# Kernel tuning notes

Measured on AMD Instinct MI355X. Metric: run time of the kernel, lower is better.

The kernel has to match this reference:

```python
import jax, jax.numpy as jnp
import numpy as np

V, E, H, O, S, N = 32000, 256, 512, 32000, 128, 256

def setup_inputs() -> dict:
    key = jax.random.key(0)
    ks = jax.random.split(key, 12)
    s = 0.05
    return {
        'x': jax.random.randint(ks[0], (N, 1), 0, V),
        'encoder_outputs': jax.random.normal(ks[1], (N, S, 2 * H), jnp.float32),
        'hidden': jax.random.normal(ks[2], (1, N, H), jnp.float32),
        'cell': jax.random.normal(ks[3], (1, N, H), jnp.float32),
        'emb': jax.random.normal(ks[4], (V, E), jnp.float32) * s,
        'W_energy': jax.random.normal(ks[5], (1, 3 * H), jnp.float32) * s,
        'b_energy': jnp.zeros((1,), jnp.float32),
        'W_ih': jax.random.normal(ks[6], (4 * H, E + 2 * H), jnp.float32) * s,
        'W_hh': jax.random.normal(ks[7], (4 * H, H), jnp.float32) * s,
        'b_ih': jnp.zeros((4 * H,), jnp.float32),
        'b_hh': jnp.zeros((4 * H,), jnp.float32),
        'W_out': jax.random.normal(ks[8], (O, H), jnp.float32) * s,
        'b_out': jnp.zeros((O,), jnp.float32),
    }

def reference(x, encoder_outputs, hidden, cell, emb, W_energy, b_energy,
              W_ih, W_hh, b_ih, b_hh, W_out, b_out):
    # Dropout is identity at inference (eval mode).
    embedding = emb[x]                      # [N,1,E]
    n, s, _ = encoder_outputs.shape
    h = hidden[0]                            # [N,H] (num_layers==1)
    h_rep = jnp.broadcast_to(h[:, None, :], (n, s, h.shape[-1]))  # [N,S,H]
    feat = jnp.concatenate([h_rep, encoder_outputs], axis=-1)     # [N,S,3H]
    energy = jax.nn.relu(feat @ W_energy.T + b_energy)            # [N,S,1]
    attention = jax.nn.softmax(energy, axis=1)                    # softmax over seq
    context = jnp.einsum('nsk,nsl->nkl', attention, encoder_outputs)  # [N,1,2H]
    lstm_in = jnp.concatenate([context, embedding], axis=-1)[:, 0, :]  # [N,E+2H]
    gates = lstm_in @ W_ih.T + b_ih + h @ W_hh.T + b_hh           # [N,4H]
    i, f, g, o = jnp.split(gates, 4, axis=-1)                     # torch gate order
    i, f, o = jax.nn.sigmoid(i), jax.nn.sigmoid(f), jax.nn.sigmoid(o)
    g = jnp.tanh(g)
    c_new = f * cell[0] + i * g
    h_new = o * jnp.tanh(c_new)
    outputs = h_new[:, None, :]                                   # [N,1,H]
    predictions = outputs @ W_out.T + b_out                       # [N,1,O]
    return predictions, h_new[None], c_new[None]
```

## Files before the change

kernel.cpp:

```cpp
#include <hip/hip_runtime.h>
#include <hip/hip_bf16.h>

#define N_ 256
#define S_ 128
#define H_ 512
#define E_ 256
#define O_ 32000
#define KZ 1792
#define GJ 2048
#define KSPLIT 4
#define KCHUNK 448
#define SSPLIT 4

typedef __attribute__((ext_vector_type(8))) short sv8;
typedef __attribute__((ext_vector_type(4))) float fv4;

__device__ __forceinline__ unsigned short f2bf(float f) {
  return __builtin_bit_cast(unsigned short, __float2bfloat16(f));
}

__device__ __forceinline__ sv8 pack8(fv4 a, fv4 b) {
  sv8 r;
  r[0] = (short)f2bf(a[0]); r[1] = (short)f2bf(a[1]);
  r[2] = (short)f2bf(a[2]); r[3] = (short)f2bf(a[3]);
  r[4] = (short)f2bf(b[0]); r[5] = (short)f2bf(b[1]);
  r[6] = (short)f2bf(b[2]); r[7] = (short)f2bf(b[3]);
  return r;
}

__global__ __launch_bounds__(256) void k_conv_wg(
    const float* __restrict__ Wih, const float* __restrict__ Whh,
    unsigned short* __restrict__ Wgbf)
{
  const int j = blockIdx.x;
  const int t = threadIdx.x;
  sv8* dst = (sv8*)(Wgbf + (size_t)j * KZ);
  if (t < 160) {
    const fv4* src = (const fv4*)(Wih + (size_t)j * 1280);
    dst[t] = pack8(src[2 * t], src[2 * t + 1]);
  } else if (t < 224) {
    const fv4* src = (const fv4*)(Whh + (size_t)j * 512);
    dst[t] = pack8(src[2 * (t - 160)], src[2 * (t - 160) + 1]);
  }
}

__global__ __launch_bounds__(512) void k_attn_part(
    const float* __restrict__ eo, const float* __restrict__ hid,
    const float* __restrict__ We, const float* __restrict__ be,
    float* __restrict__ pctx, float* __restrict__ pml)
{
  const int n = blockIdx.x;
  const int q = blockIdx.y;
  const int t = threadIdx.x;
  const int w = t >> 6;
  const int l = t & 63;

  __shared__ float s_red[8];
  __shared__ float s_m[8], s_l[8];
  __shared__ float s_ctx[8][1024];

  float hv = hid[(size_t)n * H_ + t] * We[t];
  #pragma unroll
  for (int off = 32; off >= 1; off >>= 1) hv += __shfl_xor(hv, off);
  if (l == 0) s_red[w] = hv;
  __syncthreads();
  float hWe = be[0];
  #pragma unroll
  for (int i = 0; i < 8; ++i) hWe += s_red[i];

  fv4 we0, we1, we2, we3;
  {
    const fv4* wp = (const fv4*)(We + H_);
    we0 = wp[l]; we1 = wp[l + 64]; we2 = wp[l + 128]; we3 = wp[l + 192];
  }

  float m = 0.f, lsum = 0.f;
  fv4 c0 = {0,0,0,0}, c1 = {0,0,0,0}, c2 = {0,0,0,0}, c3 = {0,0,0,0};
  const float* eob = eo + ((size_t)n * S_ + q * 32 + w * 4) * 1024;
  #pragma unroll 2
  for (int i = 0; i < 4; ++i) {
    const fv4* p = (const fv4*)(eob + (size_t)i * 1024);
    fv4 v0 = p[l], v1 = p[l + 64], v2 = p[l + 128], v3 = p[l + 192];
    float d = 0.f;
    #pragma unroll
    for (int c = 0; c < 4; ++c)
      d += v0[c]*we0[c] + v1[c]*we1[c] + v2[c]*we2[c] + v3[c]*we3[c];
    #pragma unroll
    for (int off = 32; off >= 1; off >>= 1) d += __shfl_xor(d, off);
    const float e  = fmaxf(d + hWe, 0.f);
    const float mn = fmaxf(m, e);
    const float sc = __expf(m - mn);
    const float pp = __expf(e - mn);
    lsum = lsum * sc + pp;
    #pragma unroll
    for (int c = 0; c < 4; ++c) {
      c0[c] = c0[c]*sc + pp*v0[c];
      c1[c] = c1[c]*sc + pp*v1[c];
      c2[c] = c2[c]*sc + pp*v2[c];
      c3[c] = c3[c]*sc + pp*v3[c];
    }
    m = mn;
  }
  if (l == 0) { s_m[w] = m; s_l[w] = lsum; }
  {
    fv4* sc_ = (fv4*)s_ctx[w];
    sc_[l] = c0; sc_[l+64] = c1; sc_[l+128] = c2; sc_[l+192] = c3;
  }
  __syncthreads();

  float M = s_m[0];
  #pragma unroll
  for (int i = 1; i < 8; ++i) M = fmaxf(M, s_m[i]);
  float wgt[8]; float L = 0.f;
  #pragma unroll
  for (int i = 0; i < 8; ++i) { wgt[i] = __expf(s_m[i] - M); L += wgt[i] * s_l[i]; }

  float* pc = pctx + ((size_t)(n * SSPLIT + q)) * 1024;
  for (int k = t; k < 1024; k += 512) {
    float acc = 0.f;
    #pragma unroll
    for (int i = 0; i < 8; ++i) acc += wgt[i] * s_ctx[i][k];
    pc[k] = acc;
  }
  if (t == 0) {
    pml[(n * SSPLIT + q) * 2 + 0] = M;
    pml[(n * SSPLIT + q) * 2 + 1] = L;
  }
}

__global__ __launch_bounds__(256) void k_attn_fin(
    const int* __restrict__ x, const float* __restrict__ emb,
    const float* __restrict__ hid, const float* __restrict__ pctx,
    const float* __restrict__ pml, unsigned short* __restrict__ z)
{
  const int n = blockIdx.x;
  const int t = threadIdx.x;
  float mq[SSPLIT], lq[SSPLIT];
  #pragma unroll
  for (int q = 0; q < SSPLIT; ++q) {
    mq[q] = pml[(n * SSPLIT + q) * 2 + 0];
    lq[q] = pml[(n * SSPLIT + q) * 2 + 1];
  }
  float M = mq[0];
  #pragma unroll
  for (int q = 1; q < SSPLIT; ++q) M = fmaxf(M, mq[q]);
  float wq[SSPLIT], L = 0.f;
  #pragma unroll
  for (int q = 0; q < SSPLIT; ++q) { wq[q] = __expf(mq[q] - M); L += wq[q] * lq[q]; }
  const float rL = 1.f / L;

  const fv4* p0 = (const fv4*)(pctx + (size_t)n * (SSPLIT * 1024));
  fv4 s = {0,0,0,0};
  #pragma unroll
  for (int q = 0; q < SSPLIT; ++q) {
    const fv4 v = p0[q * 256 + t];
    #pragma unroll
    for (int c = 0; c < 4; ++c) s[c] += wq[q] * v[c];
  }
  unsigned short* zr = z + (size_t)n * KZ;
  ushort4 o;
  o.x = f2bf(s[0] * rL);
  o.y = f2bf(s[1] * rL);
  o.z = f2bf(s[2] * rL);
  o.w = f2bf(s[3] * rL);
  *(ushort4*)(zr + 4*t) = o;

  zr[1024 + t] = f2bf(emb[(size_t)x[n] * E_ + t]);
  zr[1280 + t] = f2bf(hid[(size_t)n * H_ + t]);
  zr[1536 + t] = f2bf(hid[(size_t)n * H_ + 256 + t]);
}

__global__ __launch_bounds__(256) void k_gates(
    const unsigned short* __restrict__ z, const unsigned short* __restrict__ Wgbf,
    float* __restrict__ part)
{
  const int j0 = blockIdx.x * 64;
  const int n0 = blockIdx.y * 64;
  const int kc = blockIdx.z * KCHUNK;
  const int t = threadIdx.x;
  const int w = t >> 6, l = t & 63;
  const int lr = l & 15, lg = l >> 4;
  const int jb = j0 + w * 16 + lr;

  const unsigned short* arow = z + kc + 8 * lg;
  const unsigned short* wrow = Wgbf + (size_t)jb * KZ + kc + 8 * lg;

  fv4 acc[4] = {{0,0,0,0},{0,0,0,0},{0,0,0,0},{0,0,0,0}};
  #pragma unroll
  for (int s = 0; s < 14; ++s) {
    const sv8 bf = *(const sv8*)(wrow + s * 32);
    #pragma unroll
    for (int f = 0; f < 4; ++f) {
      const sv8 af = *(const sv8*)(arow + (size_t)(n0 + f*16 + lr) * KZ + s * 32);
      acc[f] = __builtin_amdgcn_mfma_f32_16x16x32_bf16(af, bf, acc[f], 0, 0, 0);
    }
  }
  float* pp = part + (size_t)blockIdx.z * (N_ * GJ);
  #pragma unroll
  for (int f = 0; f < 4; ++f) {
    #pragma unroll
    for (int r = 0; r < 4; ++r)
      pp[(size_t)(n0 + f*16 + lg*4 + r) * GJ + jb] = acc[f][r];
  }
}

__global__ __launch_bounds__(256) void k_lstm(
    const float* __restrict__ part, const float* __restrict__ cell,
    const float* __restrict__ bih, const float* __restrict__ bhh,
    float* __restrict__ hout, float* __restrict__ cout,
    unsigned short* __restrict__ hbf)
{
  const int tid = blockIdx.x * 256 + threadIdx.x;
  const int n = tid >> 9, hh = tid & 511;
  const size_t base = (size_t)n * GJ;
  float ig = bih[hh]        + bhh[hh];
  float fg = bih[512 + hh]  + bhh[512 + hh];
  float gg = bih[1024 + hh] + bhh[1024 + hh];
  float og = bih[1536 + hh] + bhh[1536 + hh];
  #pragma unroll
  for (int k = 0; k < KSPLIT; ++k) {
    const float* p = part + (size_t)k * (N_ * GJ) + base;
    ig += p[hh];
    fg += p[512 + hh];
    gg += p[1024 + hh];
    og += p[1536 + hh];
  }
  ig = 1.f / (1.f + __expf(-ig));
  fg = 1.f / (1.f + __expf(-fg));
  og = 1.f / (1.f + __expf(-og));
  gg = tanhf(gg);
  const float c = fg * cell[tid] + ig * gg;
  const float h = og * tanhf(c);
  cout[tid] = c;
  hout[tid] = h;
  hbf[tid] = f2bf(h);
}

__global__ __launch_bounds__(512, 2) void k_pred(
    const unsigned short* __restrict__ hbf, const float* __restrict__ Wout,
    const float* __restrict__ bout, float* __restrict__ pred)
{
  __shared__ unsigned short Blds[64 * 512];
  const int o0 = blockIdx.x * 64;
  const int t = threadIdx.x;

  #pragma unroll
  for (int i = 0; i < 8; ++i) {
    const int g = t + i * 512;
    const int row = g >> 6, c = g & 63;
    const fv4* src = (const fv4*)(Wout + (size_t)(o0 + row) * H_ + c * 8);
    const sv8 v = pack8(src[0], src[1]);
    *(sv8*)((char*)Blds + row * 1024 + ((c * 16) ^ ((row & 7) << 4))) = v;
  }
  __syncthreads();

  const int w = t >> 6, l = t & 63;
  const int lr = l & 15, lg = l >> 4;
  const int nr = w * 32;

  fv4 acc[2][4] = {};
  #pragma unroll
  for (int kk = 0; kk < 16; ++kk) {
    sv8 a[2];
    #pragma unroll
    for (int f = 0; f < 2; ++f)
      a[f] = *(const sv8*)(hbf + (size_t)(nr + f*16 + lr) * H_ + kk*32 + 8*lg);
    #pragma unroll
    for (int fo = 0; fo < 4; ++fo) {
      const int row = fo * 16 + lr;
      const sv8 b = *(const sv8*)((const char*)Blds + row * 1024 +
                                  ((kk*64 + lg*16) ^ ((row & 7) << 4)));
      #pragma unroll
      for (int f = 0; f < 2; ++f)
        acc[f][fo] = __builtin_amdgcn_mfma_f32_16x16x32_bf16(a[f], b, acc[f][fo], 0, 0, 0);
    }
  }
  #pragma unroll
  for (int fo = 0; fo < 4; ++fo) {
    const int oo = o0 + fo*16 + lr;
    const float bo = bout[oo];
    #pragma unroll
    for (int f = 0; f < 2; ++f) {
      #pragma unroll
      for (int r = 0; r < 4; ++r)
        pred[(size_t)(nr + f*16 + lg*4 + r) * O_ + oo] = acc[f][fo][r] + bo;
    }
  }
}

extern "C" void kernel_launch(void* const* d_in, const int* in_sizes, int n_in,
                              void* d_out, int out_size, void* d_ws, size_t ws_size,
                              hipStream_t stream) {
  const int*   x    = (const int*)  d_in[0];
  const float* eo   = (const float*)d_in[1];
  const float* hid  = (const float*)d_in[2];
  const float* cell = (const float*)d_in[3];
  const float* emb  = (const float*)d_in[4];
  const float* We   = (const float*)d_in[5];
  const float* be   = (const float*)d_in[6];
  const float* Wih  = (const float*)d_in[7];
  const float* Whh  = (const float*)d_in[8];
  const float* bih  = (const float*)d_in[9];
  const float* bhh  = (const float*)d_in[10];
  const float* Wout = (const float*)d_in[11];
  const float* bout = (const float*)d_in[12];

  float* pred = (float*)d_out;
  float* hout = pred + (size_t)N_ * O_;
  float* cout = hout + (size_t)N_ * H_;

  unsigned short* z    = (unsigned short*)d_ws;
  unsigned short* hbf  = z + (size_t)N_ * KZ;
  float* part = (float*)(hbf + (size_t)N_ * H_);
  float* pctx = part + (size_t)KSPLIT * N_ * GJ;
  float* pml  = pctx + (size_t)N_ * SSPLIT * 1024;
  unsigned short* Wgbf = (unsigned short*)(pml + 2048);

  k_conv_wg  <<<GJ, 256, 0, stream>>>(Wih, Whh, Wgbf);
  k_attn_part<<<dim3(256, SSPLIT), 512, 0, stream>>>(eo, hid, We, be, pctx, pml);
  k_attn_fin <<<256, 256, 0, stream>>>(x, emb, hid, pctx, pml, z);
  k_gates<<<dim3(32, 4, KSPLIT), 256, 0, stream>>>(z, Wgbf, part);
  k_lstm <<<512, 256, 0, stream>>>(part, cell, bih, bhh, hout, cout, hbf);
  k_pred <<<500, 512, 0, stream>>>(hbf, Wout, bout, pred);
}
```

Before: 92.16 us.

## Merge weight conversion and attention into one kernel with full-sequence blocks

Three launches (weight bf16 conversion, split attention partials, attention finalize) become one kernel. blockIdx.y selects either the attention path or the weight conversion path, which now runs as a grid-stride loop. Each attention block uses 1024 threads covering all 128 sequence positions, so the partial context/max/sum round trip through global memory and a launch disappear. In exchange, the attention grid drops from 1024 to 256 blocks, and each block needs 64KB of shared memory, which may reduce occupancy and parallelism for the bandwidth-heavy encoder read.

```diff
diff --git a/kernel.cpp b/kernel.cpp
--- a/kernel.cpp
+++ b/kernel.cpp
@@ -10,7 +10,6 @@
 #define GJ 2048
 #define KSPLIT 4
 #define KCHUNK 448
-#define SSPLIT 4
 
 typedef __attribute__((ext_vector_type(8))) short sv8;
 typedef __attribute__((ext_vector_type(4))) float fv4;
@@ -28,38 +27,40 @@
   return r;
 }
 
-__global__ __launch_bounds__(256) void k_conv_wg(
+__global__ __launch_bounds__(1024) void k_attn(
+    const int* __restrict__ x, const float* __restrict__ eo,
+    const float* __restrict__ hid, const float* __restrict__ emb,
+    const float* __restrict__ We, const float* __restrict__ be,
     const float* __restrict__ Wih, const float* __restrict__ Whh,
-    unsigned short* __restrict__ Wgbf)
-{
-  const int j = blockIdx.x;
-  const int t = threadIdx.x;
-  sv8* dst = (sv8*)(Wgbf + (size_t)j * KZ);
-  if (t < 160) {
-    const fv4* src = (const fv4*)(Wih + (size_t)j * 1280);
-    dst[t] = pack8(src[2 * t], src[2 * t + 1]);
-  } else if (t < 224) {
-    const fv4* src = (const fv4*)(Whh + (size_t)j * 512);
-    dst[t] = pack8(src[2 * (t - 160)], src[2 * (t - 160) + 1]);
-  }
-}
-
-__global__ __launch_bounds__(512) void k_attn_part(
-    const float* __restrict__ eo, const float* __restrict__ hid,
-    const float* __restrict__ We, const float* __restrict__ be,
-    float* __restrict__ pctx, float* __restrict__ pml)
-{
+    unsigned short* __restrict__ Wgbf, unsigned short* __restrict__ z)
+{
+  if (blockIdx.y == 1) {
+    const int tid = blockIdx.x * 1024 + threadIdx.x;
+    for (int g = tid; g < 2048 * 224; g += 256 * 1024) {
+      const int j = g / 224, c = g - j * 224;
+      sv8* dst = (sv8*)(Wgbf + (size_t)j * KZ);
+      if (c < 160) {
+        const fv4* src = (const fv4*)(Wih + (size_t)j * 1280);
+        dst[c] = pack8(src[2 * c], src[2 * c + 1]);
+      } else {
+        const int cc = c - 160;
+        const fv4* src = (const fv4*)(Whh + (size_t)j * 512);
+        dst[c] = pack8(src[2 * cc], src[2 * cc + 1]);
+      }
+    }
+    return;
+  }
+
   const int n = blockIdx.x;
-  const int q = blockIdx.y;
   const int t = threadIdx.x;
   const int w = t >> 6;
   const int l = t & 63;
 
-  __shared__ float s_red[8];
-  __shared__ float s_m[8], s_l[8];
-  __shared__ float s_ctx[8][1024];
-
-  float hv = hid[(size_t)n * H_ + t] * We[t];
+  __shared__ float s_red[16];
+  __shared__ float s_m[16], s_l[16];
+  __shared__ float s_ctx[16][1024];
+
+  float hv = (t < 512) ? hid[(size_t)n * H_ + t] * We[t] : 0.f;
   #pragma unroll
   for (int off = 32; off >= 1; off >>= 1) hv += __shfl_xor(hv, off);
   if (l == 0) s_red[w] = hv;
@@ -76,9 +77,9 @@
 
   float m = 0.f, lsum = 0.f;
   fv4 c0 = {0,0,0,0}, c1 = {0,0,0,0}, c2 = {0,0,0,0}, c3 = {0,0,0,0};
-  const float* eob = eo + ((size_t)n * S_ + q * 32 + w * 4) * 1024;
+  const float* eob = eo + ((size_t)n * S_ + w * 8) * 1024;
   #pragma unroll 2
-  for (int i = 0; i < 4; ++i) {
+  for (int i = 0; i < 8; ++i) {
     const fv4* p = (const fv4*)(eob + (size_t)i * 1024);
     fv4 v0 = p[l], v1 = p[l + 64], v2 = p[l + 128], v3 = p[l + 192];
     float d = 0.f;
@@ -110,64 +111,20 @@
 
   float M = s_m[0];
   #pragma unroll
-  for (int i = 1; i < 8; ++i) M = fmaxf(M, s_m[i]);
-  float wgt[8]; float L = 0.f;
-  #pragma unroll
-  for (int i = 0; i < 8; ++i) { wgt[i] = __expf(s_m[i] - M); L += wgt[i] * s_l[i]; }
-
-  float* pc = pctx + ((size_t)(n * SSPLIT + q)) * 1024;
-  for (int k = t; k < 1024; k += 512) {
-    float acc = 0.f;
-    #pragma unroll
-    for (int i = 0; i < 8; ++i) acc += wgt[i] * s_ctx[i][k];
-    pc[k] = acc;
-  }
-  if (t == 0) {
-    pml[(n * SSPLIT + q) * 2 + 0] = M;
-    pml[(n * SSPLIT + q) * 2 + 1] = L;
-  }
-}
-
-__global__ __launch_bounds__(256) void k_attn_fin(
-    const int* __restrict__ x, const float* __restrict__ emb,
-    const float* __restrict__ hid, const float* __restrict__ pctx,
-    const float* __restrict__ pml, unsigned short* __restrict__ z)
-{
-  const int n = blockIdx.x;
-  const int t = threadIdx.x;
-  float mq[SSPLIT], lq[SSPLIT];
-  #pragma unroll
-  for (int q = 0; q < SSPLIT; ++q) {
-    mq[q] = pml[(n * SSPLIT + q) * 2 + 0];
-    lq[q] = pml[(n * SSPLIT + q) * 2 + 1];
-  }
-  float M = mq[0];
-  #pragma unroll
-  for (int q = 1; q < SSPLIT; ++q) M = fmaxf(M, mq[q]);
-  float wq[SSPLIT], L = 0.f;
-  #pragma unroll
-  for (int q = 0; q < SSPLIT; ++q) { wq[q] = __expf(mq[q] - M); L += wq[q] * lq[q]; }
+  for (int i = 1; i < 16; ++i) M = fmaxf(M, s_m[i]);
+  float wgt[16]; float L = 0.f;
+  #pragma unroll
+  for (int i = 0; i < 16; ++i) { wgt[i] = __expf(s_m[i] - M); L += wgt[i] * s_l[i]; }
   const float rL = 1.f / L;
 
-  const fv4* p0 = (const fv4*)(pctx + (size_t)n * (SSPLIT * 1024));
-  fv4 s = {0,0,0,0};
-  #pragma unroll
-  for (int q = 0; q < SSPLIT; ++q) {
-    const fv4 v = p0[q * 256 + t];
-    #pragma unroll
-    for (int c = 0; c < 4; ++c) s[c] += wq[q] * v[c];
-  }
+  float acc = 0.f;
+  #pragma unroll
+  for (int i = 0; i < 16; ++i) acc += wgt[i] * s_ctx[i][t];
   unsigned short* zr = z + (size_t)n * KZ;
-  ushort4 o;
-  o.x = f2bf(s[0] * rL);
-  o.y = f2bf(s[1] * rL);
-  o.z = f2bf(s[2] * rL);
-  o.w = f2bf(s[3] * rL);
-  *(ushort4*)(zr + 4*t) = o;
-
-  zr[1024 + t] = f2bf(emb[(size_t)x[n] * E_ + t]);
-  zr[1280 + t] = f2bf(hid[(size_t)n * H_ + t]);
-  zr[1536 + t] = f2bf(hid[(size_t)n * H_ + 256 + t]);
+  zr[t] = f2bf(acc * rL);
+
+  if (t < 256)       zr[1024 + t] = f2bf(emb[(size_t)x[n] * E_ + t]);
+  else if (t < 768)  zr[1024 + t] = f2bf(hid[(size_t)n * H_ + (t - 256)]);
 }
 
 __global__ __launch_bounds__(256) void k_gates(
@@ -312,13 +269,10 @@
   unsigned short* z    = (unsigned short*)d_ws;
   unsigned short* hbf  = z + (size_t)N_ * KZ;
   float* part = (float*)(hbf + (size_t)N_ * H_);
-  float* pctx = part + (size_t)KSPLIT * N_ * GJ;
-  float* pml  = pctx + (size_t)N_ * SSPLIT * 1024;
-  unsigned short* Wgbf = (unsigned short*)(pml + 2048);
-
-  k_conv_wg  <<<GJ, 256, 0, stream>>>(Wih, Whh, Wgbf);
-  k_attn_part<<<dim3(256, SSPLIT), 512, 0, stream>>>(eo, hid, We, be, pctx, pml);
-  k_attn_fin <<<256, 256, 0, stream>>>(x, emb, hid, pctx, pml, z);
+  unsigned short* Wgbf = (unsigned short*)(part + (size_t)KSPLIT * N_ * GJ);
+
+  k_attn <<<dim3(256, 2), 1024, 0, stream>>>(x, eo, hid, emb, We, be,
+                                             Wih, Whh, Wgbf, z);
   k_gates<<<dim3(32, 4, KSPLIT), 256, 0, stream>>>(z, Wgbf, part);
   k_lstm <<<512, 256, 0, stream>>>(part, cell, bih, bhh, hout, cout, hbf);
   k_pred <<<500, 512, 0, stream>>>(hbf, Wout, bout, pred);
```

After: 88.71 us. 1.04x faster.
